# Kernel tuning notes

Hardware: AMD Instinct MI355X
Metric: run time of the kernel (lower is better)

## Reference

```python
import jax, jax.numpy as jnp
import numpy as np

B, S, H = 4, 2048, 1024
E, K, F = 8, 2, 4096


def setup_inputs() -> dict:
    key = jax.random.key(0)
    ks = jax.random.split(key, 6)
    x = jax.random.normal(ks[0], (B, S, H), dtype=jnp.float32)
    gate_w = jax.random.normal(ks[1], (H, E), dtype=jnp.float32) * 0.02
    w1 = jax.random.normal(ks[2], (E, H, F), dtype=jnp.float32) * 0.02
    b1 = jnp.zeros((E, F), dtype=jnp.float32)
    w2 = jax.random.normal(ks[3], (E, F, H), dtype=jnp.float32) * 0.02
    b2 = jnp.zeros((E, H), dtype=jnp.float32)
    return {"x": x, "gate_w": gate_w, "w1": w1, "b1": b1, "w2": w2, "b2": b2}


def reference(x, gate_w, w1, b1, w2, b2):
    # NOTE: the torch module masks expert inputs per token, but since each
    # expert's output is re-masked by the same mask, the math is exactly
    # out[t] = sum_i renorm_prob[t,i] * expert_{topk_idx[t,i]}(x[t]).
    # Dropout is identity in eval mode.
    T = B * S
    x_flat = x.reshape(T, H)

    gate_scores = x_flat @ gate_w                      # [T, E]
    gate_probs = jax.nn.softmax(gate_scores, axis=-1)  # [T, E]
    topk_vals, topk_idx = jax.lax.top_k(gate_probs, K)  # [T, K]
    topk_w = jax.nn.softmax(topk_vals, axis=-1)        # renormalize via softmax (as in source)

    # Combine weights per (token, expert): sum over top-k slots.
    onehot = jax.nn.one_hot(topk_idx, E, dtype=x.dtype)           # [T, K, E]
    comb = jnp.einsum('tk,tke->te', topk_w, onehot)               # [T, E]

    # Run all experts densely (faithful to naive module; combine masks out unrouted).
    h = jnp.einsum('th,ehf->etf', x_flat, w1) + b1[:, None, :]    # [E, T, F]
    h = jax.nn.relu(h)
    expert_out = jnp.einsum('etf,efh->eth', h, w2) + b2[:, None, :]  # [E, T, H]

    out_flat = jnp.einsum('te,eth->th', comb, expert_out)         # [T, H]
    output = out_flat.reshape(B, S, H)

    # Load-balance loss: KL(uniform || softmax(mean gate prob)), batchmean over E.
    expert_usage = gate_probs.mean(axis=0)                        # [E]
    log_sm = jax.nn.log_softmax(expert_usage, axis=0)
    uniform = jnp.full((E,), 1.0 / E, dtype=x.dtype)
    kl = jnp.sum(uniform * (jnp.log(uniform) - log_sm)) / E
    load_balance_loss = 0.01 * kl
    return output, load_balance_loss
```

## Files before the change

### kernel.cpp

```cpp
#include <hip/hip_runtime.h>
#include <stdint.h>

#define T_TOK 8192
#define HD 1024
#define NE 8
#define FD 4096
#define RALLOC 18432
#define G1 1152
#define G2 384
#define NKT1 16
#define GATE_BLOCKS 1024

typedef __attribute__((ext_vector_type(8))) short bf16x8;
typedef __attribute__((ext_vector_type(4))) float f32x4;
typedef __attribute__((ext_vector_type(4))) short s16x4;

__device__ __forceinline__ unsigned short f2bf(float f) {
  unsigned u = __builtin_bit_cast(unsigned, f);
  u += 0x7fffu + ((u >> 16) & 1u);
  return (unsigned short)(u >> 16);
}

__device__ __forceinline__ void gld_lds16(const void* g, void* l) {
  __builtin_amdgcn_global_load_lds(
      (const __attribute__((address_space(1))) void*)g,
      (__attribute__((address_space(3))) void*)l, 16, 0, 0);
}

__global__ __launch_bounds__(256) void k_transpose(const float* __restrict__ src,
                                                   unsigned short* __restrict__ dst,
                                                   int R, int C) {
  __shared__ unsigned short tile[64 * 80];
  const float* s = src + (size_t)blockIdx.z * R * C;
  unsigned short* d = dst + (size_t)blockIdx.z * R * C;
  const int r0 = blockIdx.y * 64, c0 = blockIdx.x * 64;
  const int tid = threadIdx.x;
  {
    const int r = tid >> 2, cg = (tid & 3) * 16;
    #pragma unroll
    for (int m = 0; m < 4; ++m) {
      float4 v = *(const float4*)(s + (size_t)(r0 + r) * C + c0 + cg + 4 * m);
      s16x4 pv;
      pv[0] = (short)f2bf(v.x); pv[1] = (short)f2bf(v.y);
      pv[2] = (short)f2bf(v.z); pv[3] = (short)f2bf(v.w);
      *(s16x4*)&tile[r * 80 + cg + 4 * m] = pv;
    }
  }
  __syncthreads();
  {
    const int c = tid >> 2, rg = (tid & 3) * 16;
    bf16x8 v0, v1;
    #pragma unroll
    for (int j = 0; j < 8; ++j) v0[j] = (short)tile[(rg + j) * 80 + c];
    #pragma unroll
    for (int j = 0; j < 8; ++j) v1[j] = (short)tile[(rg + 8 + j) * 80 + c];
    unsigned short* dp = d + (size_t)(c0 + c) * R + r0 + rg;
    *(bf16x8*)dp = v0;
    *(bf16x8*)(dp + 8) = v1;
  }
}

__global__ __launch_bounds__(512) void k_gating(const float* __restrict__ x,
                                                const float* __restrict__ gw,
                                                int* __restrict__ toke,
                                                float* __restrict__ tokw,
                                                int* __restrict__ counts8,
                                                double* __restrict__ part,
                                                unsigned short* __restrict__ xbf) {
  __shared__ float gwT[8 * 1024];
  __shared__ double sp[8][8];
  __shared__ int scnt[8];
  const int tid = threadIdx.x;
  const int lane = tid & 63;
  const int w = tid >> 6;
  if (tid < 8) scnt[tid] = 0;
  #pragma unroll
  for (int rep = 0; rep < 16; ++rep) {
    int idx = rep * 512 + tid;
    gwT[(idx & 7) * 1024 + (idx >> 3)] = gw[idx];
  }
  __syncthreads();

  const int t = blockIdx.x * 8 + w;
  double acc[8];
  #pragma unroll
  for (int e = 0; e < 8; ++e) acc[e] = 0.0;
  const float* xr = x + (size_t)t * HD;
  unsigned short* xbr = xbf + (size_t)t * HD;
  #pragma unroll
  for (int j = 0; j < 4; ++j) {
    const int hh = j * 256 + lane * 4;
    float4 xv = *(const float4*)(xr + hh);
    s16x4 pv;
    pv[0] = (short)f2bf(xv.x); pv[1] = (short)f2bf(xv.y);
    pv[2] = (short)f2bf(xv.z); pv[3] = (short)f2bf(xv.w);
    *(s16x4*)(xbr + hh) = pv;
    #pragma unroll
    for (int e = 0; e < 8; ++e) {
      float4 gv = *(const float4*)(gwT + e * 1024 + hh);
      acc[e] += (double)xv.x * (double)gv.x;
      acc[e] += (double)xv.y * (double)gv.y;
      acc[e] += (double)xv.z * (double)gv.z;
      acc[e] += (double)xv.w * (double)gv.w;
    }
  }
  for (int off = 32; off > 0; off >>= 1) {
    #pragma unroll
    for (int e = 0; e < 8; ++e) acc[e] += __shfl_xor(acc[e], off, 64);
  }
  double m = acc[0];
  #pragma unroll
  for (int e = 1; e < 8; ++e) m = fmax(m, acc[e]);
  double p[8], ssum = 0.0;
  #pragma unroll
  for (int e = 0; e < 8; ++e) { p[e] = exp(acc[e] - m); ssum += p[e]; }
  double inv = 1.0 / ssum;
  #pragma unroll
  for (int e = 0; e < 8; ++e) p[e] *= inv;
  int e0 = 0;
  #pragma unroll
  for (int e = 1; e < 8; ++e) if (p[e] > p[e0]) e0 = e;
  int e1 = (e0 == 0) ? 1 : 0;
  #pragma unroll
  for (int e = 0; e < 8; ++e) if (e != e0 && p[e] > p[e1]) e1 = e;
  if (lane == 0) {
    double z = exp(p[e1] - p[e0]);
    double w0 = 1.0 / (1.0 + z);
    toke[2 * t] = e0; toke[2 * t + 1] = e1;
    tokw[2 * t] = (float)w0; tokw[2 * t + 1] = (float)(z / (1.0 + z));
    atomicAdd(&scnt[e0], 1);
    atomicAdd(&scnt[e1], 1);
    #pragma unroll
    for (int e = 0; e < 8; ++e) sp[w][e] = p[e];
  }
  __syncthreads();
  if (tid < 8) {
    double s = 0.0;
    #pragma unroll
    for (int q = 0; q < 8; ++q) s += sp[q][tid];
    part[(size_t)blockIdx.x * 8 + tid] = s;
    counts8[(size_t)blockIdx.x * 8 + tid] = scnt[tid];
  }
}

__global__ __launch_bounds__(256) void k_scan(const int* __restrict__ counts8,
                                              int* __restrict__ offs,
                                              int* __restrict__ cursors,
                                              const double* __restrict__ part,
                                              float* __restrict__ loss_out,
                                              int* __restrict__ rowmap,
                                              float* __restrict__ roww) {
  __shared__ double su[8];
  __shared__ int soffs[9];
  __shared__ int scnt[8];
  const int tid = threadIdx.x;
  const int e = tid >> 5, sub = tid & 31;
  double s = 0.0;
  int c = 0;
  for (int b = sub; b < GATE_BLOCKS; b += 32) {
    s += part[(size_t)b * 8 + e];
    c += counts8[(size_t)b * 8 + e];
  }
  for (int off = 16; off > 0; off >>= 1) {
    s += __shfl_xor(s, off, 64);
    c += __shfl_xor(c, off, 64);
  }
  if (sub == 0) { su[e] = s; scnt[e] = c; }
  __syncthreads();
  if (tid == 0) {
    int o = 0;
    for (int i = 0; i < 8; ++i) {
      soffs[i] = o; offs[i] = o; cursors[i * 16] = o;
      o += ((scnt[i] + 255) >> 8) << 8;
    }
    soffs[8] = o; offs[8] = o;
    double u[8], mx = -1e300;
    for (int i = 0; i < 8; ++i) { u[i] = su[i] / 8192.0; mx = fmax(mx, u[i]); }
    double se = 0.0;
    for (int i = 0; i < 8; ++i) se += exp(u[i] - mx);
    double lse = mx + log(se);
    double kl = 0.0;
    const double lu = log(0.125);
    for (int i = 0; i < 8; ++i) kl += 0.125 * (lu - (u[i] - lse));
    kl /= 8.0;
    loss_out[0] = (float)(0.01 * kl);
  }
  __syncthreads();
  for (int i = 0; i < 8; ++i) {
    int s0 = soffs[i] + scnt[i];
    int en = soffs[i + 1];
    for (int k = s0 + tid; k < en; k += 256) { rowmap[k] = 2 * T_TOK; roww[k] = 0.f; }
  }
}

__global__ __launch_bounds__(256) void k_scatter(const int* __restrict__ toke,
                                                 const float* __restrict__ tokw,
                                                 int* __restrict__ cursors,
                                                 int* __restrict__ rowmap,
                                                 float* __restrict__ roww) {
  const int t = blockIdx.x * 256 + threadIdx.x;
  const int lane = threadIdx.x & 63;
  #pragma unroll
  for (int k = 0; k < 2; ++k) {
    int e = toke[2 * t + k];
    float wv = tokw[2 * t + k];
    for (int ex = 0; ex < 8; ++ex) {
      unsigned long long mask = __ballot(e == ex);
      if (e == ex) {
        int leader = __ffsll((unsigned long long)mask) - 1;
        int rank = __popcll(mask & ((1ull << lane) - 1ull));
        int base = 0;
        if (lane == leader) base = atomicAdd(&cursors[ex * 16], __popcll(mask));
        base = __shfl(base, leader, 64);
        rowmap[base + rank] = 2 * t + k;
        roww[base + rank] = wv;
      }
    }
  }
}

#define RDA(buf, mh) do { _Pragma("unroll") for (int m_ = 0; m_ < 4; ++m_) { \
  af[m_][0] = *(const bf16x8*)(lds + (buf) * 65536 + wmOff + (mh) * 8192 + aoff[m_][0]); \
  af[m_][1] = *(const bf16x8*)(lds + (buf) * 65536 + wmOff + (mh) * 8192 + aoff[m_][1]); } } while (0)

#define RDB(buf, nh, B) do { _Pragma("unroll") for (int nf_ = 0; nf_ < 2; ++nf_) { \
  B[nf_][0] = *(const bf16x8*)(lds + (buf) * 65536 + wnOff + (nh) * 4096 + boff[nf_][0]); \
  B[nf_][1] = *(const bf16x8*)(lds + (buf) * 65536 + wnOff + (nh) * 4096 + boff[nf_][1]); } } while (0)

#define MMA(mh, nh, B) do { _Pragma("unroll") for (int m_ = 0; m_ < 4; ++m_) \
  _Pragma("unroll") for (int nf_ = 0; nf_ < 2; ++nf_) \
  _Pragma("unroll") for (int kh_ = 0; kh_ < 2; ++kh_) \
    acc[(mh) * 4 + m_][(nh) * 2 + nf_] = __builtin_amdgcn_mfma_f32_16x16x32_bf16( \
        af[m_][kh_], B[nf_][kh_], acc[(mh) * 4 + m_][(nh) * 2 + nf_], 0, 0, 0); } while (0)

#define SYNC_PRE() do { __builtin_amdgcn_sched_barrier(0); __builtin_amdgcn_s_barrier(); \
  asm volatile("s_waitcnt lgkmcnt(0)" ::: "memory"); __builtin_amdgcn_sched_barrier(0); \
  __builtin_amdgcn_s_setprio(1); } while (0)

#define SYNC_POST() do { __builtin_amdgcn_s_setprio(0); __builtin_amdgcn_sched_barrier(0); \
  __builtin_amdgcn_s_barrier(); __builtin_amdgcn_sched_barrier(0); } while (0)

#define SYNC_POST_VM() do { __builtin_amdgcn_s_setprio(0); __builtin_amdgcn_sched_barrier(0); \
  asm volatile("s_waitcnt vmcnt(4)" ::: "memory"); __builtin_amdgcn_sched_barrier(0); \
  __builtin_amdgcn_s_barrier(); __builtin_amdgcn_sched_barrier(0); } while (0)

#define FRAG_OFFSETS256() \
  int aoff[4][2], boff[2][2]; \
  { \
    const int kg = (lane >> 4) << 4; \
    _Pragma("unroll") \
    for (int m = 0; m < 4; ++m) { \
      int r = m * 16 + (lane & 15); \
      _Pragma("unroll") \
      for (int kh = 0; kh < 2; ++kh) \
        aoff[m][kh] = r * 128 + ((kh * 64 + kg) ^ ((r & 7) << 4)); \
    } \
    _Pragma("unroll") \
    for (int nf = 0; nf < 2; ++nf) { \
      int r = (wn & 1) * 64 + nf * 16 + (lane & 15); \
      _Pragma("unroll") \
      for (int kh = 0; kh < 2; ++kh) \
        boff[nf][kh] = r * 128 + ((kh * 64 + kg) ^ ((r & 7) << 4)); \
    } \
  }

__global__ __launch_bounds__(512, 2) void k_gemm1(const unsigned short* __restrict__ xbf,
                                                  const unsigned short* __restrict__ w1t,
                                                  const float* __restrict__ b1,
                                                  const int* __restrict__ rowmap,
                                                  const int* __restrict__ offs,
                                                  unsigned short* __restrict__ hbuf) {
  __shared__ char lds[131072];
  const int id = blockIdx.x;
  const int sid = (id & 7) * 144 + (id >> 3);
  const int bx = sid & 15, by = sid >> 4;
  const int row0 = by * 256;
  if (row0 >= offs[8]) return;
  int e = 0;
  #pragma unroll
  for (int i = 1; i < 8; ++i) if (row0 >= offs[i]) e = i;
  const int n0 = bx * 256;
  const int tid = threadIdx.x;
  const int lane = tid & 63;
  const int wid = tid >> 6;
  const int wm = wid >> 2, wn = wid & 3;

  const int rl = tid >> 3;
  const int cbs = ((tid & 7) << 4) ^ ((rl & 7) << 4);
  const char* pA[2][2];
  #pragma unroll
  for (int h = 0; h < 2; ++h)
    #pragma unroll
    for (int l = 0; l < 2; ++l) {
      int tok = rowmap[row0 + h * 128 + l * 64 + rl] >> 1;
      pA[h][l] = (const char*)xbf + (size_t)tok * 2048 + cbs;
    }
  const char* pB00 = (const char*)w1t + (size_t)e * ((size_t)FD * HD * 2) +
                     (size_t)(n0 + rl) * 2048 + cbs;
  const int stw = wid * 1024;

#define STA1(buf, h, kt) do { \
  gld_lds16(pA[h][0] + (size_t)(kt) * 128, lds + (buf) * 65536 + (h) * 16384 + stw); \
  gld_lds16(pA[h][1] + (size_t)(kt) * 128, lds + (buf) * 65536 + (h) * 16384 + 8192 + stw); } while (0)
#define STB1(buf, h, kt) do { \
  gld_lds16(pB00 + (size_t)(h) * 128 * 2048 + (size_t)(kt) * 128, \
            lds + (buf) * 65536 + 32768 + (h) * 16384 + stw); \
  gld_lds16(pB00 + ((size_t)(h) * 128 + 64) * 2048 + (size_t)(kt) * 128, \
            lds + (buf) * 65536 + 32768 + (h) * 16384 + 8192 + stw); } while (0)

  FRAG_OFFSETS256();
  const int wmOff = wm * 16384;
  const int wnOff = 32768 + (wn >> 1) * 16384;

  f32x4 acc[8][4];
  #pragma unroll
  for (int a = 0; a < 8; ++a)
    #pragma unroll
    for (int b = 0; b < 4; ++b) acc[a][b] = (f32x4){0.f, 0.f, 0.f, 0.f};
  bf16x8 af[4][2], b0r[2][2], b1r[2][2];

  STA1(0, 0, 0); STA1(0, 1, 0); STB1(0, 0, 0); STB1(0, 1, 0);
  STB1(1, 0, 1); STB1(1, 1, 1);
  asm volatile("s_waitcnt vmcnt(4)" ::: "memory");
  __builtin_amdgcn_sched_barrier(0);
  __builtin_amdgcn_s_barrier();
  __builtin_amdgcn_sched_barrier(0);

  #pragma unroll 1
  for (int i = 0; i < NKT1 / 2; ++i) {
    const int k1 = 2 * i + 1, k2 = 2 * i + 2, k3 = 2 * i + 3;
    RDA(0, 0); RDB(0, 0, b0r); STA1(1, 0, k1); SYNC_PRE(); MMA(0, 0, b0r); SYNC_POST();
    RDB(0, 1, b1r);            STA1(1, 1, k1); SYNC_PRE(); MMA(0, 1, b1r); SYNC_POST();
    RDA(0, 1);                 STB1(0, 0, k2); SYNC_PRE(); MMA(1, 1, b1r); SYNC_POST();
                               STB1(0, 1, k2); SYNC_PRE(); MMA(1, 0, b0r); SYNC_POST_VM();
    RDA(1, 0); RDB(1, 0, b0r); STA1(0, 0, k2); SYNC_PRE(); MMA(0, 0, b0r); SYNC_POST();
    RDB(1, 1, b1r);            STA1(0, 1, k2); SYNC_PRE(); MMA(0, 1, b1r); SYNC_POST();
    RDA(1, 1);                 STB1(1, 0, k3); SYNC_PRE(); MMA(1, 1, b1r); SYNC_POST();
                               STB1(1, 1, k3); SYNC_PRE(); MMA(1, 0, b0r); SYNC_POST_VM();
  }

  asm volatile("s_waitcnt vmcnt(0)" ::: "memory");
  __builtin_amdgcn_sched_barrier(0);
  __syncthreads();
  #pragma unroll
  for (int na = 0; na < 4; ++na) {
    int c = wn * 64 + (na >> 1) * 32 + (na & 1) * 16 + (lane & 15);
    float bias = b1[(size_t)e * FD + n0 + c];
    #pragma unroll
    for (int ma = 0; ma < 8; ++ma) {
      #pragma unroll
      for (int j = 0; j < 4; ++j) {
        int r = wm * 128 + (ma >> 2) * 64 + (ma & 3) * 16 + ((lane >> 4) << 2) + j;
        float v = fmaxf(acc[ma][na][j] + bias, 0.f);
        *(unsigned short*)(lds + r * 512 + ((c * 2) ^ ((r & 7) << 4))) = f2bf(v);
      }
    }
  }
  __syncthreads();
  #pragma unroll
  for (int s = 0; s < 16; ++s) {
    int flat = s * 512 + tid;
    int r = flat >> 5, ch = flat & 31;
    bf16x8 v = *(const bf16x8*)(lds + r * 512 + ((ch * 16) ^ ((r & 7) << 4)));
    *(bf16x8*)((char*)hbuf + (size_t)(row0 + r) * 8192 + (size_t)n0 * 2 + ch * 16) = v;
  }
#undef STA1
#undef STB1
}

__global__ __launch_bounds__(512, 2) void k_gemm2(const unsigned short* __restrict__ hbuf,
                                                  const unsigned short* __restrict__ w2t,
                                                  const float* __restrict__ b2,
                                                  const int* __restrict__ rowmap,
                                                  const float* __restrict__ roww,
                                                  const int* __restrict__ offs,
                                                  float* __restrict__ out2,
                                                  float* __restrict__ psplit) {
  __shared__ char lds[131072];
  const int id = blockIdx.x;
  int bx, by, kt0, niter, jj = -1;
  if (id < 256) {
    const int sid = (id & 7) * 32 + (id >> 3);
    bx = sid & 3; by = sid >> 2;
    kt0 = 0; niter = 32;
  } else {
    jj = ((id - 256) & 7) * 16 + ((id - 256) >> 3);
    const int t = 256 + (jj >> 2);
    const int nT2 = (offs[8] >> 8) * 4;
    if (t >= nT2) return;
    bx = t & 3; by = t >> 2;
    kt0 = (jj & 3) * 16; niter = 8;
  }
  const int row0 = by * 256;
  int e = 0;
  #pragma unroll
  for (int i = 1; i < 8; ++i) if (row0 >= offs[i]) e = i;
  const int n0 = bx * 256;
  const int tid = threadIdx.x;
  const int lane = tid & 63;
  const int wid = tid >> 6;
  const int wm = wid >> 2, wn = wid & 3;

  const int rl = tid >> 3;
  const int cbs = ((tid & 7) << 4) ^ ((rl & 7) << 4);
  const char* pA00 = (const char*)hbuf + (size_t)(row0 + rl) * 8192 + cbs;
  const char* pB00 = (const char*)w2t + (size_t)e * ((size_t)HD * FD * 2) +
                     (size_t)(n0 + rl) * 8192 + cbs;
  const int stw = wid * 1024;

#define STA2(buf, h, kt) do { \
  gld_lds16(pA00 + (size_t)(h) * 128 * 8192 + (size_t)(kt) * 128, \
            lds + (buf) * 65536 + (h) * 16384 + stw); \
  gld_lds16(pA00 + ((size_t)(h) * 128 + 64) * 8192 + (size_t)(kt) * 128, \
            lds + (buf) * 65536 + (h) * 16384 + 8192 + stw); } while (0)
#define STB2(buf, h, kt) do { \
  gld_lds16(pB00 + (size_t)(h) * 128 * 8192 + (size_t)(kt) * 128, \
            lds + (buf) * 65536 + 32768 + (h) * 16384 + stw); \
  gld_lds16(pB00 + ((size_t)(h) * 128 + 64) * 8192 + (size_t)(kt) * 128, \
            lds + (buf) * 65536 + 32768 + (h) * 16384 + 8192 + stw); } while (0)

  FRAG_OFFSETS256();
  const int wmOff = wm * 16384;
  const int wnOff = 32768 + (wn >> 1) * 16384;

  f32x4 acc[8][4];
  #pragma unroll
  for (int a = 0; a < 8; ++a)
    #pragma unroll
    for (int b = 0; b < 4; ++b) acc[a][b] = (f32x4){0.f, 0.f, 0.f, 0.f};
  bf16x8 af[4][2], b0r[2][2], b1r[2][2];

  STA2(0, 0, kt0); STA2(0, 1, kt0); STB2(0, 0, kt0); STB2(0, 1, kt0);
  STB2(1, 0, kt0 + 1); STB2(1, 1, kt0 + 1);
  asm volatile("s_waitcnt vmcnt(4)" ::: "memory");
  __builtin_amdgcn_sched_barrier(0);
  __builtin_amdgcn_s_barrier();
  __builtin_amdgcn_sched_barrier(0);

  #pragma unroll 1
  for (int i = 0; i < niter; ++i) {
    const int k1 = kt0 + 2 * i + 1, k2 = kt0 + 2 * i + 2, k3 = kt0 + 2 * i + 3;
    RDA(0, 0); RDB(0, 0, b0r); STA2(1, 0, k1); SYNC_PRE(); MMA(0, 0, b0r); SYNC_POST();
    RDB(0, 1, b1r);            STA2(1, 1, k1); SYNC_PRE(); MMA(0, 1, b1r); SYNC_POST();
    RDA(0, 1);                 STB2(0, 0, k2); SYNC_PRE(); MMA(1, 1, b1r); SYNC_POST();
                               STB2(0, 1, k2); SYNC_PRE(); MMA(1, 0, b0r); SYNC_POST_VM();
    RDA(1, 0); RDB(1, 0, b0r); STA2(0, 0, k2); SYNC_PRE(); MMA(0, 0, b0r); SYNC_POST();
    RDB(1, 1, b1r);            STA2(0, 1, k2); SYNC_PRE(); MMA(0, 1, b1r); SYNC_POST();
    RDA(1, 1);                 STB2(1, 0, k3); SYNC_PRE(); MMA(1, 1, b1r); SYNC_POST();
                               STB2(1, 1, k3); SYNC_PRE(); MMA(1, 0, b0r); SYNC_POST_VM();
  }

  asm volatile("s_waitcnt vmcnt(0)" ::: "memory");
  __builtin_amdgcn_sched_barrier(0);
  if (jj < 0) {
    #pragma unroll
    for (int ma = 0; ma < 8; ++ma) {
      #pragma unroll
      for (int j = 0; j < 4; ++j) {
        int r = wm * 128 + (ma >> 2) * 64 + (ma & 3) * 16 + ((lane >> 4) << 2) + j;
        int rm = rowmap[row0 + r];
        float wr = roww[row0 + r];
        float* orow = out2 + (size_t)rm * 1024 + n0;
        #pragma unroll
        for (int na = 0; na < 4; ++na) {
          int c = wn * 64 + (na >> 1) * 32 + (na & 1) * 16 + (lane & 15);
          orow[c] = (acc[ma][na][j] + b2[(size_t)e * HD + n0 + c]) * wr;
        }
      }
    }
  } else {
    float* ps = psplit + (size_t)jj * 65536;
    #pragma unroll
    for (int ma = 0; ma < 8; ++ma) {
      #pragma unroll
      for (int j = 0; j < 4; ++j) {
        int r = wm * 128 + (ma >> 2) * 64 + (ma & 3) * 16 + ((lane >> 4) << 2) + j;
        #pragma unroll
        for (int na = 0; na < 4; ++na) {
          int c = wn * 64 + (na >> 1) * 32 + (na & 1) * 16 + (lane & 15);
          ps[r * 256 + c] = acc[ma][na][j];
        }
      }
    }
  }
#undef STA2
#undef STB2
}

__global__ __launch_bounds__(512) void k_fix2(const float* __restrict__ psplit,
                                              const int* __restrict__ offs,
                                              const float* __restrict__ b2,
                                              const int* __restrict__ rowmap,
                                              const float* __restrict__ roww,
                                              float* __restrict__ out2) {
  const int nT2 = (offs[8] >> 8) * 4;
  const int t = 256 + blockIdx.x;
  if (t >= nT2) return;
  const int by = t >> 2, bx = t & 3;
  const int row0 = by * 256, n0 = bx * 256;
  int e = 0;
  #pragma unroll
  for (int i = 1; i < 8; ++i) if (row0 >= offs[i]) e = i;
  const float* ps = psplit + (size_t)blockIdx.x * 4 * 65536;
  const int cg = (threadIdx.x & 63) * 4;
  const int r0t = threadIdx.x >> 6;
  float4 bb = *(const float4*)(b2 + (size_t)e * HD + n0 + cg);
  for (int rr = 0; rr < 32; ++rr) {
    int r = rr * 8 + r0t;
    int rm = rowmap[row0 + r];
    float wr = roww[row0 + r];
    float4 s0 = *(const float4*)(ps + 0 * 65536 + r * 256 + cg);
    float4 s1 = *(const float4*)(ps + 1 * 65536 + r * 256 + cg);
    float4 s2 = *(const float4*)(ps + 2 * 65536 + r * 256 + cg);
    float4 s3 = *(const float4*)(ps + 3 * 65536 + r * 256 + cg);
    float4 o;
    o.x = wr * (s0.x + s1.x + s2.x + s3.x + bb.x);
    o.y = wr * (s0.y + s1.y + s2.y + s3.y + bb.y);
    o.z = wr * (s0.z + s1.z + s2.z + s3.z + bb.z);
    o.w = wr * (s0.w + s1.w + s2.w + s3.w + bb.w);
    *(float4*)(out2 + (size_t)rm * 1024 + n0 + cg) = o;
  }
}

__global__ __launch_bounds__(256) void k_combine(const float* __restrict__ out2,
                                                 float* __restrict__ out) {
  const int t = blockIdx.x;
  const int i = threadIdx.x * 4;
  float4 a = *(const float4*)(out2 + (size_t)(2 * t) * 1024 + i);
  float4 b = *(const float4*)(out2 + (size_t)(2 * t + 1) * 1024 + i);
  float4 r;
  r.x = a.x + b.x; r.y = a.y + b.y; r.z = a.z + b.z; r.w = a.w + b.w;
  *(float4*)(out + (size_t)t * 1024 + i) = r;
}

extern "C" void kernel_launch(void* const* d_in, const int* in_sizes, int n_in,
                              void* d_out, int out_size, void* d_ws, size_t ws_size,
                              hipStream_t stream) {
  const float* x = (const float*)d_in[0];
  const float* gw = (const float*)d_in[1];
  const float* w1 = (const float*)d_in[2];
  const float* b1 = (const float*)d_in[3];
  const float* w2 = (const float*)d_in[4];
  const float* b2 = (const float*)d_in[5];
  float* out = (float*)d_out;

  char* ws = (char*)d_ws;
  size_t o = 0;
  unsigned short* w2t = (unsigned short*)(ws + o); o += (size_t)NE * HD * FD * 2;
  unsigned short* hbuf = (unsigned short*)(ws + o); o += (size_t)RALLOC * FD * 2;
  unsigned short* w1t = (unsigned short*)(ws + o);
  size_t w1t_off = o; o += (size_t)NE * FD * HD * 2;
  unsigned short* xbf = (unsigned short*)(ws + o); o += (size_t)T_TOK * HD * 2;
  int* rowmap = (int*)(ws + o); o += (size_t)RALLOC * 4;
  float* roww = (float*)(ws + o); o += (size_t)RALLOC * 4;
  int* toke = (int*)(ws + o); o += (size_t)T_TOK * 2 * 4;
  float* tokw = (float*)(ws + o); o += (size_t)T_TOK * 2 * 4;
  double* part = (double*)(ws + o); o += (size_t)GATE_BLOCKS * 8 * 8;
  int* counts8 = (int*)(ws + o); o += (size_t)GATE_BLOCKS * 8 * 4;
  int* ctrl = (int*)(ws + o); o += 1024;
  int* offs = ctrl;
  int* cursors = ctrl + 64;
  float* psplit = (float*)(ws + o); o += (size_t)128 * 65536 * 4;
  float* out2 = (float*)(ws + w1t_off);

  k_transpose<<<dim3(FD / 64, HD / 64, NE), 256, 0, stream>>>(w1, w1t, HD, FD);
  k_transpose<<<dim3(HD / 64, FD / 64, NE), 256, 0, stream>>>(w2, w2t, FD, HD);
  k_gating<<<GATE_BLOCKS, 512, 0, stream>>>(x, gw, toke, tokw, counts8, part, xbf);
  k_scan<<<1, 256, 0, stream>>>(counts8, offs, cursors, part, out + (size_t)T_TOK * HD,
                                rowmap, roww);
  k_scatter<<<T_TOK / 256, 256, 0, stream>>>(toke, tokw, cursors, rowmap, roww);
  k_gemm1<<<G1, 512, 0, stream>>>(xbf, w1t, b1, rowmap, offs, hbuf);
  k_gemm2<<<G2, 512, 0, stream>>>(hbuf, w2t, b2, rowmap, roww, offs, out2, psplit);
  k_fix2<<<32, 512, 0, stream>>>(psplit, offs, b2, rowmap, roww, out2);
  k_combine<<<T_TOK, 256, 0, stream>>>(out2, out);
}
```

Measured before the change: 472.9 us.

## Merge weight transposes, remap gemm1 tiles per XCD, widen gemm2 split-K tail

```diff
diff --git a/kernel.cpp b/kernel.cpp
--- a/kernel.cpp
+++ b/kernel.cpp
@@ -7,7 +7,6 @@
 #define FD 4096
 #define RALLOC 18432
 #define G1 1152
-#define G2 384
 #define NKT1 16
 #define GATE_BLOCKS 1024
 
@@ -27,19 +26,30 @@
       (__attribute__((address_space(3))) void*)l, 16, 0, 0);
 }
 
-__global__ __launch_bounds__(256) void k_transpose(const float* __restrict__ src,
-                                                   unsigned short* __restrict__ dst,
-                                                   int R, int C) {
+__global__ __launch_bounds__(256) void k_transpose2(const float* __restrict__ w1,
+                                                    const float* __restrict__ w2,
+                                                    unsigned short* __restrict__ w1t,
+                                                    unsigned short* __restrict__ w2t) {
   __shared__ unsigned short tile[64 * 80];
-  const float* s = src + (size_t)blockIdx.z * R * C;
-  unsigned short* d = dst + (size_t)blockIdx.z * R * C;
-  const int r0 = blockIdx.y * 64, c0 = blockIdx.x * 64;
+  const int i = blockIdx.x;
+  const float* src;
+  unsigned short* dst;
+  int R, C, r0, c0;
+  if (i < 8192) {
+    const int e = i >> 10, rem = i & 1023;
+    R = HD; C = FD; r0 = (rem >> 6) << 6; c0 = (rem & 63) << 6;
+    src = w1 + (size_t)e * R * C; dst = w1t + (size_t)e * R * C;
+  } else {
+    const int e = (i - 8192) >> 10, rem = (i - 8192) & 1023;
+    R = FD; C = HD; r0 = (rem >> 4) << 6; c0 = (rem & 15) << 6;
+    src = w2 + (size_t)e * R * C; dst = w2t + (size_t)e * R * C;
+  }
   const int tid = threadIdx.x;
   {
     const int r = tid >> 2, cg = (tid & 3) * 16;
     #pragma unroll
     for (int m = 0; m < 4; ++m) {
-      float4 v = *(const float4*)(s + (size_t)(r0 + r) * C + c0 + cg + 4 * m);
+      float4 v = *(const float4*)(src + (size_t)(r0 + r) * C + c0 + cg + 4 * m);
       s16x4 pv;
       pv[0] = (short)f2bf(v.x); pv[1] = (short)f2bf(v.y);
       pv[2] = (short)f2bf(v.z); pv[3] = (short)f2bf(v.w);
@@ -54,7 +64,7 @@
     for (int j = 0; j < 8; ++j) v0[j] = (short)tile[(rg + j) * 80 + c];
     #pragma unroll
     for (int j = 0; j < 8; ++j) v1[j] = (short)tile[(rg + 8 + j) * 80 + c];
-    unsigned short* dp = d + (size_t)(c0 + c) * R + r0 + rg;
+    unsigned short* dp = dst + (size_t)(c0 + c) * R + r0 + rg;
     *(bf16x8*)dp = v0;
     *(bf16x8*)(dp + 8) = v1;
   }
@@ -272,14 +282,15 @@
                                                   unsigned short* __restrict__ hbuf) {
   __shared__ char lds[131072];
   const int id = blockIdx.x;
-  const int sid = (id & 7) * 144 + (id >> 3);
-  const int bx = sid & 15, by = sid >> 4;
-  const int row0 = by * 256;
+  const int j = id >> 3, xcd = id & 7;
+  const int rt = xcd + 8 * (j >> 4);
+  const int nb = j & 15;
+  const int row0 = rt * 256;
   if (row0 >= offs[8]) return;
   int e = 0;
   #pragma unroll
   for (int i = 1; i < 8; ++i) if (row0 >= offs[i]) e = i;
-  const int n0 = bx * 256;
+  const int n0 = nb * 256;
   const int tid = threadIdx.x;
   const int lane = tid & 63;
   const int wid = tid >> 6;
@@ -349,9 +360,9 @@
     #pragma unroll
     for (int ma = 0; ma < 8; ++ma) {
       #pragma unroll
-      for (int j = 0; j < 4; ++j) {
-        int r = wm * 128 + (ma >> 2) * 64 + (ma & 3) * 16 + ((lane >> 4) << 2) + j;
-        float v = fmaxf(acc[ma][na][j] + bias, 0.f);
+      for (int j2 = 0; j2 < 4; ++j2) {
+        int r = wm * 128 + (ma >> 2) * 64 + (ma & 3) * 16 + ((lane >> 4) << 2) + j2;
+        float v = fmaxf(acc[ma][na][j2] + bias, 0.f);
         *(unsigned short*)(lds + r * 512 + ((c * 2) ^ ((r & 7) << 4))) = f2bf(v);
       }
     }
@@ -375,7 +386,8 @@
                                                   const float* __restrict__ roww,
                                                   const int* __restrict__ offs,
                                                   float* __restrict__ out2,
-                                                  float* __restrict__ psplit) {
+                                                  float* __restrict__ psplit,
+                                                  int nss) {
   __shared__ char lds[131072];
   const int id = blockIdx.x;
   int bx, by, kt0, niter, jj = -1;
@@ -384,12 +396,17 @@
     bx = sid & 3; by = sid >> 2;
     kt0 = 0; niter = 32;
   } else {
-    jj = ((id - 256) & 7) * 16 + ((id - 256) >> 3);
-    const int t = 256 + (jj >> 2);
+    const int jid = id - 256;
+    const int jpx = 4 << nss;
+    const int q = (jid & 7) * jpx + (jid >> 3);
+    const int t = 256 + (q >> nss);
     const int nT2 = (offs[8] >> 8) * 4;
     if (t >= nT2) return;
     bx = t & 3; by = t >> 2;
-    kt0 = (jj & 3) * 16; niter = 8;
+    const int seg = q & ((1 << nss) - 1);
+    kt0 = seg << (6 - nss);
+    niter = 32 >> nss;
+    jj = q;
   }
   const int row0 = by * 256;
   int e = 0;
@@ -456,15 +473,15 @@
     #pragma unroll
     for (int ma = 0; ma < 8; ++ma) {
       #pragma unroll
-      for (int j = 0; j < 4; ++j) {
-        int r = wm * 128 + (ma >> 2) * 64 + (ma & 3) * 16 + ((lane >> 4) << 2) + j;
+      for (int j2 = 0; j2 < 4; ++j2) {
+        int r = wm * 128 + (ma >> 2) * 64 + (ma & 3) * 16 + ((lane >> 4) << 2) + j2;
         int rm = rowmap[row0 + r];
         float wr = roww[row0 + r];
         float* orow = out2 + (size_t)rm * 1024 + n0;
         #pragma unroll
         for (int na = 0; na < 4; ++na) {
           int c = wn * 64 + (na >> 1) * 32 + (na & 1) * 16 + (lane & 15);
-          orow[c] = (acc[ma][na][j] + b2[(size_t)e * HD + n0 + c]) * wr;
+          orow[c] = (acc[ma][na][j2] + b2[(size_t)e * HD + n0 + c]) * wr;
         }
       }
     }
@@ -473,12 +490,12 @@
     #pragma unroll
     for (int ma = 0; ma < 8; ++ma) {
       #pragma unroll
-      for (int j = 0; j < 4; ++j) {
-        int r = wm * 128 + (ma >> 2) * 64 + (ma & 3) * 16 + ((lane >> 4) << 2) + j;
+      for (int j2 = 0; j2 < 4; ++j2) {
+        int r = wm * 128 + (ma >> 2) * 64 + (ma & 3) * 16 + ((lane >> 4) << 2) + j2;
         #pragma unroll
         for (int na = 0; na < 4; ++na) {
           int c = wn * 64 + (na >> 1) * 32 + (na & 1) * 16 + (lane & 15);
-          ps[r * 256 + c] = acc[ma][na][j];
+          ps[r * 256 + c] = acc[ma][na][j2];
         }
       }
     }
@@ -492,7 +509,8 @@
                                               const float* __restrict__ b2,
                                               const int* __restrict__ rowmap,
                                               const float* __restrict__ roww,
-                                              float* __restrict__ out2) {
+                                              float* __restrict__ out2,
+                                              int nsegs) {
   const int nT2 = (offs[8] >> 8) * 4;
   const int t = 256 + blockIdx.x;
   if (t >= nT2) return;
@@ -501,7 +519,7 @@
   int e = 0;
   #pragma unroll
   for (int i = 1; i < 8; ++i) if (row0 >= offs[i]) e = i;
-  const float* ps = psplit + (size_t)blockIdx.x * 4 * 65536;
+  const float* ps = psplit + (size_t)blockIdx.x * nsegs * 65536;
   const int cg = (threadIdx.x & 63) * 4;
   const int r0t = threadIdx.x >> 6;
   float4 bb = *(const float4*)(b2 + (size_t)e * HD + n0 + cg);
@@ -509,15 +527,13 @@
     int r = rr * 8 + r0t;
     int rm = rowmap[row0 + r];
     float wr = roww[row0 + r];
-    float4 s0 = *(const float4*)(ps + 0 * 65536 + r * 256 + cg);
-    float4 s1 = *(const float4*)(ps + 1 * 65536 + r * 256 + cg);
-    float4 s2 = *(const float4*)(ps + 2 * 65536 + r * 256 + cg);
-    float4 s3 = *(const float4*)(ps + 3 * 65536 + r * 256 + cg);
+    float4 s = bb;
+    for (int k = 0; k < nsegs; ++k) {
+      float4 v = *(const float4*)(ps + (size_t)k * 65536 + r * 256 + cg);
+      s.x += v.x; s.y += v.y; s.z += v.z; s.w += v.w;
+    }
     float4 o;
-    o.x = wr * (s0.x + s1.x + s2.x + s3.x + bb.x);
-    o.y = wr * (s0.y + s1.y + s2.y + s3.y + bb.y);
-    o.z = wr * (s0.z + s1.z + s2.z + s3.z + bb.z);
-    o.w = wr * (s0.w + s1.w + s2.w + s3.w + bb.w);
+    o.x = wr * s.x; o.y = wr * s.y; o.z = wr * s.z; o.w = wr * s.w;
     *(float4*)(out2 + (size_t)rm * 1024 + n0 + cg) = o;
   }
 }
@@ -560,17 +576,19 @@
   int* ctrl = (int*)(ws + o); o += 1024;
   int* offs = ctrl;
   int* cursors = ctrl + 64;
-  float* psplit = (float*)(ws + o); o += (size_t)128 * 65536 * 4;
+  float* psplit = (float*)(ws + o);
+  const int nss = (ws_size >= o + (size_t)256 * 65536 * 4) ? 3 : 2;
+  const int nsegs = 1 << nss;
+  const int G2 = 256 + 32 * nsegs;
   float* out2 = (float*)(ws + w1t_off);
 
-  k_transpose<<<dim3(FD / 64, HD / 64, NE), 256, 0, stream>>>(w1, w1t, HD, FD);
-  k_transpose<<<dim3(HD / 64, FD / 64, NE), 256, 0, stream>>>(w2, w2t, FD, HD);
+  k_transpose2<<<16384, 256, 0, stream>>>(w1, w2, w1t, w2t);
   k_gating<<<GATE_BLOCKS, 512, 0, stream>>>(x, gw, toke, tokw, counts8, part, xbf);
   k_scan<<<1, 256, 0, stream>>>(counts8, offs, cursors, part, out + (size_t)T_TOK * HD,
                                 rowmap, roww);
   k_scatter<<<T_TOK / 256, 256, 0, stream>>>(toke, tokw, cursors, rowmap, roww);
   k_gemm1<<<G1, 512, 0, stream>>>(xbf, w1t, b1, rowmap, offs, hbuf);
-  k_gemm2<<<G2, 512, 0, stream>>>(hbuf, w2t, b2, rowmap, roww, offs, out2, psplit);
-  k_fix2<<<32, 512, 0, stream>>>(psplit, offs, b2, rowmap, roww, out2);
+  k_gemm2<<<G2, 512, 0, stream>>>(hbuf, w2t, b2, rowmap, roww, offs, out2, psplit, nss);
+  k_fix2<<<32, 512, 0, stream>>>(psplit, offs, b2, rowmap, roww, out2, nsegs);
   k_combine<<<T_TOK, 256, 0, stream>>>(out2, out);
 }
```

After: 537.4 us. 13.7% more time.
